# Kernel tuning notes

Measured on AMD Instinct MI355X. Metric: run time of the kernel, lower is better.

Reference implementation:

```python
import math
import jax, jax.numpy as jnp
import numpy as np

N_HEAD = 16

def setup_inputs() -> dict:
    key = jax.random.key(0)
    ks = jax.random.split(key, 6)
    B, T, C = 4, 2048, 1024
    s = 1.0 / math.sqrt(C)
    return {
        "x": jax.random.normal(ks[0], (B, T, C), jnp.float32),
        "Wq": jax.random.normal(ks[1], (C, C), jnp.float32) * s,
        "bq": jnp.zeros((C,), jnp.float32),
        "Wk": jax.random.normal(ks[2], (C, C), jnp.float32) * s,
        "bk": jnp.zeros((C,), jnp.float32),
        "Wv": jax.random.normal(ks[3], (C, C), jnp.float32) * s,
        "bv": jnp.zeros((C,), jnp.float32),
        "Wp": jax.random.normal(ks[4], (C, C), jnp.float32) * s,
        "bp": jnp.zeros((C,), jnp.float32),
    }

def reference(x, Wq, bq, Wk, bk, Wv, bv, Wp, bp):
    B, T, C = x.shape
    H = N_HEAD
    D = C // H
    # QKV projections -> (B, H, T, D)
    def heads(y):
        return y.reshape(B, T, H, D).transpose(0, 2, 1, 3)
    q = heads(x @ Wq + bq)
    k = heads(x @ Wk + bk)
    v = heads(x @ Wv + bv)
    # scaled causal attention logits (B, H, T, T)
    att = jnp.einsum('bhqd,bhkd->bhqk', q, k) * (1.0 / math.sqrt(D))
    causal = jnp.tril(jnp.ones((T, T), bool))
    att = jnp.where(causal, att, jnp.float32(-jnp.inf))
    att = jax.nn.softmax(att, axis=-1)
    y = jnp.einsum('bhqk,bhkd->bhqd', att, v)  # (B, H, T, D)
    y = y.transpose(0, 2, 1, 3).reshape(B, T, C)
    return y @ Wp + bp
```

## Files before the change

kernel.cpp:

```cpp
#include <hip/hip_runtime.h>
#include <hip/hip_bf16.h>

#define T_SEQ 2048
#define C_DIM 1024
#define H_NUM 16
#define D_HEAD 64
#define B_BATCH 4
#define M_ROWS (B_BATCH * T_SEQ)

typedef __attribute__((ext_vector_type(8))) short short8;
typedef __attribute__((ext_vector_type(4))) short short4v;
typedef __attribute__((ext_vector_type(4))) float float4v;
typedef __attribute__((ext_vector_type(4))) int int4v;

#define GLOAD_LDS16(gp, lp)                                                              \
    __builtin_amdgcn_global_load_lds(                                                    \
        (const __attribute__((address_space(1))) void*)(gp),                             \
        (__attribute__((address_space(3))) void*)(lp), 16, 0, 0)

static __device__ inline short f2bf(float f) {
    __hip_bfloat16 h = __float2bfloat16(f);
    return *reinterpret_cast<short*>(&h);
}

__global__ void k_convert_x(const float* __restrict__ x, short* __restrict__ xb, int n4) {
    int i = blockIdx.x * blockDim.x + threadIdx.x;
    int stride = gridDim.x * blockDim.x;
    for (; i < n4; i += stride) {
        float4v v = reinterpret_cast<const float4v*>(x)[i];
        short4v o;
        o[0] = f2bf(v[0]); o[1] = f2bf(v[1]); o[2] = f2bf(v[2]); o[3] = f2bf(v[3]);
        reinterpret_cast<short4v*>(xb)[i] = o;
    }
}

__global__ void k_transpose_w(const float* __restrict__ Wq, const float* __restrict__ Wk,
                              const float* __restrict__ Wv, const float* __restrict__ Wp,
                              short* __restrict__ out) {
    __shared__ float tile[32][33];
    const float* W = (blockIdx.z == 0) ? Wq : (blockIdx.z == 1) ? Wk : (blockIdx.z == 2) ? Wv : Wp;
    short* o = out + (size_t)blockIdx.z * C_DIM * C_DIM;
    int x = blockIdx.x * 32 + threadIdx.x;
    int y0 = blockIdx.y * 32;
    for (int i = 0; i < 32; i += 8)
        tile[threadIdx.y + i][threadIdx.x] = W[(size_t)(y0 + threadIdx.y + i) * C_DIM + x];
    __syncthreads();
    int xo = y0 + threadIdx.x;
    int yo0 = blockIdx.x * 32;
    for (int i = 0; i < 32; i += 8)
        o[(size_t)(yo0 + threadIdx.y + i) * C_DIM + xo] = f2bf(tile[threadIdx.x][threadIdx.y + i]);
}

template <int MODE>
__global__ __launch_bounds__(256) void k_gemm(const short* __restrict__ A,
                                              const short* __restrict__ Bt,
                                              const float* __restrict__ bias,
                                              void* __restrict__ outp) {
    __shared__ short As[128][32];
    __shared__ short Bs[128][32];
    const int tid  = threadIdx.x;
    const int lane = tid & 63;
    const int w    = tid >> 6;
    const int wm   = w >> 1, wn = w & 1;
    const int bm   = blockIdx.y, bn = blockIdx.x;
    const int lrow = lane & 15;
    const int kgrp = lane >> 4;

    const int srow = lane >> 2;
    const int scol = (lane & 3) * 8;
    const short* gA = A  + (size_t)(bm * 128 + w * 32 + srow) * C_DIM + scol;
    const short* gB = Bt + (size_t)(bn * 128 + w * 32 + srow) * C_DIM + scol;
    short* lA0 = &As[w * 32][0];
    short* lA1 = &As[w * 32 + 16][0];
    short* lB0 = &Bs[w * 32][0];
    short* lB1 = &Bs[w * 32 + 16][0];

    float4v acc[4][4];
    const float4v fz = {0.f, 0.f, 0.f, 0.f};
    for (int i = 0; i < 4; ++i)
        for (int n = 0; n < 4; ++n) acc[i][n] = fz;

    for (int kt = 0; kt < C_DIM / 32; ++kt) {
        const int ko = kt * 32;
        GLOAD_LDS16(gA + ko,               lA0);
        GLOAD_LDS16(gA + ko + 16 * C_DIM, lA1);
        GLOAD_LDS16(gB + ko,               lB0);
        GLOAD_LDS16(gB + ko + 16 * C_DIM, lB1);
        __syncthreads();
        short8 af[4], bf[4];
#pragma unroll
        for (int i = 0; i < 4; ++i)
            af[i] = *reinterpret_cast<const short8*>(&As[wm * 64 + i * 16 + lrow][kgrp * 8]);
#pragma unroll
        for (int n = 0; n < 4; ++n)
            bf[n] = *reinterpret_cast<const short8*>(&Bs[wn * 64 + n * 16 + lrow][kgrp * 8]);
#pragma unroll
        for (int i = 0; i < 4; ++i)
#pragma unroll
            for (int n = 0; n < 4; ++n)
                acc[i][n] = __builtin_amdgcn_mfma_f32_16x16x32_bf16(af[i], bf[n], acc[i][n], 0, 0, 0);
        __syncthreads();
    }

    int cols[4];
    float bias_v[4];
#pragma unroll
    for (int n = 0; n < 4; ++n) {
        cols[n] = bn * 128 + wn * 64 + n * 16 + lrow;
        bias_v[n] = bias[cols[n]];
    }
#pragma unroll
    for (int i = 0; i < 4; ++i) {
        int m0 = bm * 128 + wm * 64 + i * 16 + kgrp * 4;
#pragma unroll
        for (int n = 0; n < 4; ++n) {
#pragma unroll
            for (int r = 0; r < 4; ++r) {
                float v = acc[i][n][r] + bias_v[n];
                int mm = m0 + r;
                if constexpr (MODE == 3) {
                    reinterpret_cast<float*>(outp)[(size_t)mm * C_DIM + cols[n]] = v;
                } else {
                    int bidx = mm >> 11, t = mm & 2047;
                    int hh = cols[n] >> 6, d = cols[n] & 63;
                    short* o = reinterpret_cast<short*>(outp);
                    if constexpr (MODE == 0) v *= 0.18033688f;
                    size_t idx;
                    if constexpr (MODE == 2)
                        idx = (((size_t)(bidx * H_NUM + hh)) * D_HEAD + d) * T_SEQ + t;
                    else
                        idx = (((size_t)(bidx * H_NUM + hh)) * T_SEQ + t) * D_HEAD + d;
                    o[idx] = f2bf(v);
                }
            }
        }
    }
}

__global__ __launch_bounds__(256) void k_attn(const short* __restrict__ qb,
                                              const short* __restrict__ kb,
                                              const short* __restrict__ vtb,
                                              short* __restrict__ yb) {
    __shared__ short p_lds[4][16][72];
    const int tid  = threadIdx.x;
    const int lane = tid & 63, w = tid >> 6;
    const int lrow = lane & 15, kgrp = lane >> 4;
    const int bh = blockIdx.y;
    const int b = bh >> 4, h = bh & 15;
    const float4v fz = {0.f, 0.f, 0.f, 0.f};
    const float THR = 8.0f;

#pragma unroll 1
    for (int phase = 0; phase < 2; ++phase) {
        const int qj = (phase == 0) ? (31 - (int)blockIdx.x) : (int)blockIdx.x;
        const int q0 = qj * 64;
        const int qrow = q0 + w * 16;

        short8 qf[2];
        {
            const short* qbase = qb + ((size_t)bh * T_SEQ + qrow + lrow) * D_HEAD + kgrp * 8;
            qf[0] = *reinterpret_cast<const short8*>(qbase);
            qf[1] = *reinterpret_cast<const short8*>(qbase + 32);
        }

        float m_r[4], l_p[4];
        float4v acc[4];
        for (int r = 0; r < 4; ++r) { m_r[r] = -__builtin_huge_valf(); l_p[r] = 0.f; }
        for (int n = 0; n < 4; ++n) acc[n] = fz;

        const int ntiles = qj + 1;
        for (int kt = 0; kt < ntiles; ++kt) {
            const int k0 = kt * 64;
            float4v s[4];
            for (int n = 0; n < 4; ++n) s[n] = fz;
            const short* kbase = kb + ((size_t)bh * T_SEQ + k0 + lrow) * D_HEAD + kgrp * 8;
#pragma unroll
            for (int n = 0; n < 4; ++n) {
                const short* kp = kbase + (size_t)n * 16 * D_HEAD;
                short8 kf0 = *reinterpret_cast<const short8*>(kp);
                short8 kf1 = *reinterpret_cast<const short8*>(kp + 32);
                s[n] = __builtin_amdgcn_mfma_f32_16x16x32_bf16(qf[0], kf0, s[n], 0, 0, 0);
                s[n] = __builtin_amdgcn_mfma_f32_16x16x32_bf16(qf[1], kf1, s[n], 0, 0, 0);
            }
            const short* vbase = vtb + ((size_t)bh * D_HEAD + lrow) * T_SEQ + k0 + kgrp * 8;
            short8 vf0[4], vf1[4];
#pragma unroll
            for (int n = 0; n < 4; ++n) {
                const short* vp = vbase + (size_t)n * 16 * T_SEQ;
                vf0[n] = *reinterpret_cast<const short8*>(vp);
                vf1[n] = *reinterpret_cast<const short8*>(vp + 32);
            }
            if (kt == ntiles - 1) {
#pragma unroll
                for (int n = 0; n < 4; ++n) {
                    int kabs = k0 + n * 16 + lrow;
#pragma unroll
                    for (int r = 0; r < 4; ++r) {
                        int qabs = qrow + kgrp * 4 + r;
                        if (kabs > qabs) s[n][r] = -__builtin_huge_valf();
                    }
                }
            }
            float tm[4];
#pragma unroll
            for (int r = 0; r < 4; ++r) {
                float t = fmaxf(fmaxf(s[0][r], s[1][r]), fmaxf(s[2][r], s[3][r]));
                t = fmaxf(t, __shfl_xor(t, 1));
                t = fmaxf(t, __shfl_xor(t, 2));
                t = fmaxf(t, __shfl_xor(t, 4));
                t = fmaxf(t, __shfl_xor(t, 8));
                tm[r] = t;
            }
            int grow = (tm[0] > m_r[0] + THR) | (tm[1] > m_r[1] + THR) |
                       (tm[2] > m_r[2] + THR) | (tm[3] > m_r[3] + THR);
            if (__any(grow)) {
#pragma unroll
                for (int r = 0; r < 4; ++r) {
                    float mnew = fmaxf(m_r[r], tm[r]);
                    float sc = exp2f(m_r[r] - mnew);
                    m_r[r] = mnew;
                    l_p[r] *= sc;
#pragma unroll
                    for (int n = 0; n < 4; ++n) acc[n][r] *= sc;
                }
            }
#pragma unroll
            for (int n = 0; n < 4; ++n)
#pragma unroll
                for (int r = 0; r < 4; ++r) {
                    float p = exp2f(s[n][r] - m_r[r]);
                    s[n][r] = p;
                    l_p[r] += p;
                }

#pragma unroll
            for (int n = 0; n < 4; ++n)
#pragma unroll
                for (int r = 0; r < 4; ++r)
                    p_lds[w][kgrp * 4 + r][n * 16 + lrow] = f2bf(s[n][r]);

            short8 pa[2];
            pa[0] = *reinterpret_cast<const short8*>(&p_lds[w][lrow][kgrp * 8]);
            pa[1] = *reinterpret_cast<const short8*>(&p_lds[w][lrow][32 + kgrp * 8]);
#pragma unroll
            for (int n = 0; n < 4; ++n) {
                acc[n] = __builtin_amdgcn_mfma_f32_16x16x32_bf16(pa[0], vf0[n], acc[n], 0, 0, 0);
                acc[n] = __builtin_amdgcn_mfma_f32_16x16x32_bf16(pa[1], vf1[n], acc[n], 0, 0, 0);
            }
        }

#pragma unroll
        for (int r = 0; r < 4; ++r) {
            float t = l_p[r];
            t += __shfl_xor(t, 1);
            t += __shfl_xor(t, 2);
            t += __shfl_xor(t, 4);
            t += __shfl_xor(t, 8);
            float inv = 1.0f / t;
            int trow = qrow + kgrp * 4 + r;
            size_t base = ((size_t)b * T_SEQ + trow) * C_DIM + h * D_HEAD;
#pragma unroll
            for (int n = 0; n < 4; ++n)
                yb[base + n * 16 + lrow] = f2bf(acc[n][r] * inv);
        }
    }
}

extern "C" void kernel_launch(void* const* d_in, const int* in_sizes, int n_in,
                              void* d_out, int out_size, void* d_ws, size_t ws_size,
                              hipStream_t stream) {
    const float* x  = (const float*)d_in[0];
    const float* Wq = (const float*)d_in[1];
    const float* bq = (const float*)d_in[2];
    const float* Wk = (const float*)d_in[3];
    const float* bk = (const float*)d_in[4];
    const float* Wv = (const float*)d_in[5];
    const float* bv = (const float*)d_in[6];
    const float* Wp = (const float*)d_in[7];
    const float* bp = (const float*)d_in[8];

    char* ws = (char*)d_ws;
    short* xb = (short*)(ws);
    short* wt = (short*)(ws + (size_t)(16 << 20));
    short* qb = (short*)(ws + (size_t)(24 << 20));
    short* kb = (short*)(ws + (size_t)(40 << 20));
    short* vt = (short*)(ws + (size_t)(56 << 20));

    k_convert_x<<<2048, 256, 0, stream>>>(x, xb, M_ROWS * C_DIM / 4);
    k_transpose_w<<<dim3(32, 32, 4), dim3(32, 8), 0, stream>>>(Wq, Wk, Wv, Wp, wt);

    k_gemm<0><<<dim3(8, 64), 256, 0, stream>>>(xb, wt,                bq, (void*)qb);
    k_gemm<1><<<dim3(8, 64), 256, 0, stream>>>(xb, wt + (1u << 20),   bk, (void*)kb);
    k_gemm<2><<<dim3(8, 64), 256, 0, stream>>>(xb, wt + (2u << 20),   bv, (void*)vt);

    k_attn<<<dim3(16, 64), 256, 0, stream>>>(qb, kb, vt, xb);

    k_gemm<3><<<dim3(8, 64), 256, 0, stream>>>(xb, wt + (3u << 20), bp, d_out);
}
```

Measured before the change: 490.5 us.

## Fuse QKV projections into one GEMM launch and software-pipeline QK^T in attention

The three separate Q/K/V projection GEMM launches become one launch with a 24-column grid. Each block picks its bias, output buffer and layout from its column-block index, and the transposed weights are read as one contiguous 3C x C matrix. This cuts launch overhead and fills the GPU with more blocks per wave. In attention, the QK^T MFMAs for the next key tile are issued before the PV MFMAs of the current tile, so the next K loads and score math can overlap softmax and PV work, at the cost of extra register pressure.

```diff
diff --git a/kernel.cpp b/kernel.cpp
--- a/kernel.cpp
+++ b/kernel.cpp
@@ -51,11 +51,14 @@
         o[(size_t)(yo0 + threadIdx.y + i) * C_DIM + xo] = f2bf(tile[threadIdx.x][threadIdx.y + i]);
 }
 
-template <int MODE>
-__global__ __launch_bounds__(256) void k_gemm(const short* __restrict__ A,
-                                              const short* __restrict__ Bt,
-                                              const float* __restrict__ bias,
-                                              void* __restrict__ outp) {
+__global__ __launch_bounds__(256) void k_gemm_qkv(const short* __restrict__ A,
+                                                  const short* __restrict__ Bt,
+                                                  const float* __restrict__ bq,
+                                                  const float* __restrict__ bk,
+                                                  const float* __restrict__ bv,
+                                                  short* __restrict__ qo,
+                                                  short* __restrict__ ko,
+                                                  short* __restrict__ vo) {
     __shared__ short As[128][32];
     __shared__ short Bs[128][32];
     const int tid  = threadIdx.x;
@@ -81,11 +84,11 @@
         for (int n = 0; n < 4; ++n) acc[i][n] = fz;
 
     for (int kt = 0; kt < C_DIM / 32; ++kt) {
-        const int ko = kt * 32;
-        GLOAD_LDS16(gA + ko,               lA0);
-        GLOAD_LDS16(gA + ko + 16 * C_DIM, lA1);
-        GLOAD_LDS16(gB + ko,               lB0);
-        GLOAD_LDS16(gB + ko + 16 * C_DIM, lB1);
+        const int ko_ = kt * 32;
+        GLOAD_LDS16(gA + ko_,               lA0);
+        GLOAD_LDS16(gA + ko_ + 16 * C_DIM, lA1);
+        GLOAD_LDS16(gB + ko_,               lB0);
+        GLOAD_LDS16(gB + ko_ + 16 * C_DIM, lB1);
         __syncthreads();
         short8 af[4], bf[4];
 #pragma unroll
@@ -102,6 +105,89 @@
         __syncthreads();
     }
 
+    const int m = bn >> 3;
+    const float* bias = (m == 0) ? bq : (m == 1) ? bk : bv;
+    short* o = (m == 0) ? qo : (m == 1) ? ko : vo;
+    int cols[4];
+    float bias_v[4];
+#pragma unroll
+    for (int n = 0; n < 4; ++n) {
+        cols[n] = (bn & 7) * 128 + wn * 64 + n * 16 + lrow;
+        bias_v[n] = bias[cols[n]];
+    }
+#pragma unroll
+    for (int i = 0; i < 4; ++i) {
+        int m0 = bm * 128 + wm * 64 + i * 16 + kgrp * 4;
+#pragma unroll
+        for (int n = 0; n < 4; ++n) {
+            int hh = cols[n] >> 6, d = cols[n] & 63;
+#pragma unroll
+            for (int r = 0; r < 4; ++r) {
+                float v = acc[i][n][r] + bias_v[n];
+                int mm = m0 + r;
+                int bidx = mm >> 11, t = mm & 2047;
+                if (m == 0) v *= 0.18033688f;
+                size_t idx;
+                if (m == 2)
+                    idx = (((size_t)(bidx * H_NUM + hh)) * D_HEAD + d) * T_SEQ + t;
+                else
+                    idx = (((size_t)(bidx * H_NUM + hh)) * T_SEQ + t) * D_HEAD + d;
+                o[idx] = f2bf(v);
+            }
+        }
+    }
+}
+
+__global__ __launch_bounds__(256) void k_gemm_proj(const short* __restrict__ A,
+                                                   const short* __restrict__ Bt,
+                                                   const float* __restrict__ bias,
+                                                   float* __restrict__ outp) {
+    __shared__ short As[128][32];
+    __shared__ short Bs[128][32];
+    const int tid  = threadIdx.x;
+    const int lane = tid & 63;
+    const int w    = tid >> 6;
+    const int wm   = w >> 1, wn = w & 1;
+    const int bm   = blockIdx.y, bn = blockIdx.x;
+    const int lrow = lane & 15;
+    const int kgrp = lane >> 4;
+
+    const int srow = lane >> 2;
+    const int scol = (lane & 3) * 8;
+    const short* gA = A  + (size_t)(bm * 128 + w * 32 + srow) * C_DIM + scol;
+    const short* gB = Bt + (size_t)(bn * 128 + w * 32 + srow) * C_DIM + scol;
+    short* lA0 = &As[w * 32][0];
+    short* lA1 = &As[w * 32 + 16][0];
+    short* lB0 = &Bs[w * 32][0];
+    short* lB1 = &Bs[w * 32 + 16][0];
+
+    float4v acc[4][4];
+    const float4v fz = {0.f, 0.f, 0.f, 0.f};
+    for (int i = 0; i < 4; ++i)
+        for (int n = 0; n < 4; ++n) acc[i][n] = fz;
+
+    for (int kt = 0; kt < C_DIM / 32; ++kt) {
+        const int ko_ = kt * 32;
+        GLOAD_LDS16(gA + ko_,               lA0);
+        GLOAD_LDS16(gA + ko_ + 16 * C_DIM, lA1);
+        GLOAD_LDS16(gB + ko_,               lB0);
+        GLOAD_LDS16(gB + ko_ + 16 * C_DIM, lB1);
+        __syncthreads();
+        short8 af[4], bf[4];
+#pragma unroll
+        for (int i = 0; i < 4; ++i)
+            af[i] = *reinterpret_cast<const short8*>(&As[wm * 64 + i * 16 + lrow][kgrp * 8]);
+#pragma unroll
+        for (int n = 0; n < 4; ++n)
+            bf[n] = *reinterpret_cast<const short8*>(&Bs[wn * 64 + n * 16 + lrow][kgrp * 8]);
+#pragma unroll
+        for (int i = 0; i < 4; ++i)
+#pragma unroll
+            for (int n = 0; n < 4; ++n)
+                acc[i][n] = __builtin_amdgcn_mfma_f32_16x16x32_bf16(af[i], bf[n], acc[i][n], 0, 0, 0);
+        __syncthreads();
+    }
+
     int cols[4];
     float bias_v[4];
 #pragma unroll
@@ -113,27 +199,10 @@
     for (int i = 0; i < 4; ++i) {
         int m0 = bm * 128 + wm * 64 + i * 16 + kgrp * 4;
 #pragma unroll
-        for (int n = 0; n < 4; ++n) {
-#pragma unroll
-            for (int r = 0; r < 4; ++r) {
-                float v = acc[i][n][r] + bias_v[n];
-                int mm = m0 + r;
-                if constexpr (MODE == 3) {
-                    reinterpret_cast<float*>(outp)[(size_t)mm * C_DIM + cols[n]] = v;
-                } else {
-                    int bidx = mm >> 11, t = mm & 2047;
-                    int hh = cols[n] >> 6, d = cols[n] & 63;
-                    short* o = reinterpret_cast<short*>(outp);
-                    if constexpr (MODE == 0) v *= 0.18033688f;
-                    size_t idx;
-                    if constexpr (MODE == 2)
-                        idx = (((size_t)(bidx * H_NUM + hh)) * D_HEAD + d) * T_SEQ + t;
-                    else
-                        idx = (((size_t)(bidx * H_NUM + hh)) * T_SEQ + t) * D_HEAD + d;
-                    o[idx] = f2bf(v);
-                }
-            }
-        }
+        for (int n = 0; n < 4; ++n)
+#pragma unroll
+            for (int r = 0; r < 4; ++r)
+                outp[(size_t)(m0 + r) * C_DIM + cols[n]] = acc[i][n][r] + bias_v[n];
     }
 }
 
@@ -165,15 +234,14 @@
 
         float m_r[4], l_p[4];
         float4v acc[4];
+        float4v s[4];
         for (int r = 0; r < 4; ++r) { m_r[r] = -__builtin_huge_valf(); l_p[r] = 0.f; }
-        for (int n = 0; n < 4; ++n) acc[n] = fz;
+        for (int n = 0; n < 4; ++n) { acc[n] = fz; s[n] = fz; }
 
         const int ntiles = qj + 1;
-        for (int kt = 0; kt < ntiles; ++kt) {
-            const int k0 = kt * 64;
-            float4v s[4];
-            for (int n = 0; n < 4; ++n) s[n] = fz;
-            const short* kbase = kb + ((size_t)bh * T_SEQ + k0 + lrow) * D_HEAD + kgrp * 8;
+
+        {
+            const short* kbase = kb + ((size_t)bh * T_SEQ + 0 + lrow) * D_HEAD + kgrp * 8;
 #pragma unroll
             for (int n = 0; n < 4; ++n) {
                 const short* kp = kbase + (size_t)n * 16 * D_HEAD;
@@ -182,6 +250,10 @@
                 s[n] = __builtin_amdgcn_mfma_f32_16x16x32_bf16(qf[0], kf0, s[n], 0, 0, 0);
                 s[n] = __builtin_amdgcn_mfma_f32_16x16x32_bf16(qf[1], kf1, s[n], 0, 0, 0);
             }
+        }
+
+        for (int kt = 0; kt < ntiles; ++kt) {
+            const int k0 = kt * 64;
             const short* vbase = vtb + ((size_t)bh * D_HEAD + lrow) * T_SEQ + k0 + kgrp * 8;
             short8 vf0[4], vf1[4];
 #pragma unroll
@@ -229,15 +301,23 @@
 #pragma unroll
                 for (int r = 0; r < 4; ++r) {
                     float p = exp2f(s[n][r] - m_r[r]);
-                    s[n][r] = p;
                     l_p[r] += p;
+                    p_lds[w][kgrp * 4 + r][n * 16 + lrow] = f2bf(p);
                 }
 
-#pragma unroll
-            for (int n = 0; n < 4; ++n)
-#pragma unroll
-                for (int r = 0; r < 4; ++r)
-                    p_lds[w][kgrp * 4 + r][n * 16 + lrow] = f2bf(s[n][r]);
+            if (kt + 1 < ntiles) {
+                const short* kbase = kb + ((size_t)bh * T_SEQ + (kt + 1) * 64 + lrow) * D_HEAD + kgrp * 8;
+#pragma unroll
+                for (int n = 0; n < 4; ++n) {
+                    const short* kp = kbase + (size_t)n * 16 * D_HEAD;
+                    short8 kf0 = *reinterpret_cast<const short8*>(kp);
+                    short8 kf1 = *reinterpret_cast<const short8*>(kp + 32);
+                    float4v t = fz;
+                    t = __builtin_amdgcn_mfma_f32_16x16x32_bf16(qf[0], kf0, t, 0, 0, 0);
+                    t = __builtin_amdgcn_mfma_f32_16x16x32_bf16(qf[1], kf1, t, 0, 0, 0);
+                    s[n] = t;
+                }
+            }
 
             short8 pa[2];
             pa[0] = *reinterpret_cast<const short8*>(&p_lds[w][lrow][kgrp * 8]);
@@ -289,11 +369,9 @@
     k_convert_x<<<2048, 256, 0, stream>>>(x, xb, M_ROWS * C_DIM / 4);
     k_transpose_w<<<dim3(32, 32, 4), dim3(32, 8), 0, stream>>>(Wq, Wk, Wv, Wp, wt);
 
-    k_gemm<0><<<dim3(8, 64), 256, 0, stream>>>(xb, wt,                bq, (void*)qb);
-    k_gemm<1><<<dim3(8, 64), 256, 0, stream>>>(xb, wt + (1u << 20),   bk, (void*)kb);
-    k_gemm<2><<<dim3(8, 64), 256, 0, stream>>>(xb, wt + (2u << 20),   bv, (void*)vt);
+    k_gemm_qkv<<<dim3(24, 64), 256, 0, stream>>>(xb, wt, bq, bk, bv, qb, kb, vt);
 
     k_attn<<<dim3(16, 64), 256, 0, stream>>>(qb, kb, vt, xb);
 
-    k_gemm<3><<<dim3(8, 64), 256, 0, stream>>>(xb, wt + (3u << 20), bp, d_out);
-}
+    k_gemm_proj<<<dim3(8, 64), 256, 0, stream>>>(xb, wt + (3u << 20), bp, (float*)d_out);
+}
```

After: 484.8 us. No clear change (-1.2%).
